# Kernel optimization log

Hardware: AMD Instinct MI355X
Metric: run time of the kernel (lower is better)

Reference implementation:

```python
import jax, jax.numpy as jnp
import numpy as np

B, T, D_MODEL = 256, 200, 2048
D_KEY, D_VAL = 128, 128


def setup_inputs() -> dict:
    key = jax.random.key(0)
    k_q, k_mask, k_wq, k_wk, k_wv = jax.random.split(key, 5)
    q = jax.random.normal(k_q, (B, T, D_MODEL), dtype=jnp.float32)
    pad_mask = jax.random.randint(k_mask, (B, 1, T), 0, 2, dtype=jnp.int32)
    # ensure key 0 is never padded so every causal row has >=1 valid key (no NaN softmax)
    pad_mask = pad_mask.at[:, :, 0].set(0)
    s = 1.0 / np.sqrt(D_MODEL)
    Wq = jax.random.normal(k_wq, (D_KEY, D_MODEL), dtype=jnp.float32) * s
    Wk = jax.random.normal(k_wk, (D_KEY, D_MODEL), dtype=jnp.float32) * s
    Wv = jax.random.normal(k_wv, (D_VAL, D_MODEL), dtype=jnp.float32) * s
    return {"q": q, "pad_mask": pad_mask, "Wq": Wq, "Wk": Wk, "Wv": Wv}


def reference(q, pad_mask, Wq, Wk, Wv):
    # self-attention: kv = q
    T_ = q.shape[1]
    C = q.shape[-1]  # note: original scales by d_model, not d_key
    Q = jnp.einsum('btc,kc->btk', q, Wq)   # [B,T,d_key]
    K = jnp.einsum('btc,kc->btk', q, Wk)   # [B,T,d_key]
    V = jnp.einsum('btc,vc->btv', q, Wv)   # [B,T,d_val]
    W = jnp.einsum('bqk,btk->bqt', Q, K) / jnp.sqrt(jnp.asarray(C, q.dtype))  # [B,T,T]
    tril = jnp.tril(jnp.ones((T_, T_), dtype=jnp.bool_))
    neg_inf = jnp.asarray(-jnp.inf, W.dtype)
    W = jnp.where(tril[None, :, :], W, neg_inf)          # causal mask
    W = jnp.where(pad_mask == 1, neg_inf, W)             # padding mask (broadcast [B,1,T])
    W = jax.nn.softmax(W, axis=-1)
    # dropout p=0.0 / eval mode -> identity
    return jnp.einsum('bqt,btv->bqv', W, V)              # [B,T,d_val]
```

## Files before the change

kernel.cpp:

```cpp
#include <hip/hip_runtime.h>

typedef __bf16 bf16x8 __attribute__((ext_vector_type(8)));
typedef __bf16 bf16x4 __attribute__((ext_vector_type(4)));
typedef float  f32x4  __attribute__((ext_vector_type(4)));

#define MFMA16(a,b,c) __builtin_amdgcn_mfma_f32_16x16x32_bf16((a),(b),(c),0,0,0)

constexpr int B_ = 256, T_ = 200, DM = 2048, DK = 128;
constexpr int VT_STRIDE = 208;

constexpr size_t OFF_W = 0;
constexpr size_t OFF_Q = 1572864;
constexpr size_t OFF_K = OFF_Q + 13107200;
constexpr size_t OFF_V = OFF_K + 13107200;

#define GLOAD_LDS16(G, L)                                                     \
  __builtin_amdgcn_global_load_lds(                                           \
      (const __attribute__((address_space(1))) void*)(G),                     \
      (__attribute__((address_space(3))) void*)(L), 16, 0, 0)

__global__ __launch_bounds__(256) void wconv_kernel(const float* __restrict__ Wq,
                                                    const float* __restrict__ Wk,
                                                    const float* __restrict__ Wv,
                                                    __bf16* __restrict__ Wcat) {
  int idx = (blockIdx.x * 256 + threadIdx.x) * 4;
  int sel = idx >> 18;
  const float* base = (sel == 0) ? Wq : (sel == 1) ? Wk : Wv;
  float4 f = *(const float4*)(base + (idx - (sel << 18)));
  bf16x4 o;
  o[0] = (__bf16)f.x; o[1] = (__bf16)f.y; o[2] = (__bf16)f.z; o[3] = (__bf16)f.w;
  *(bf16x4*)(Wcat + idx) = o;
}

__global__ __launch_bounds__(256) void proj_kernel(const float* __restrict__ q,
                                                   const __bf16* __restrict__ Wcat,
                                                   __bf16* __restrict__ Qo,
                                                   __bf16* __restrict__ Ko,
                                                   __bf16* __restrict__ Vt) {
  __shared__ alignas(16) char smem[65536];

  const int tid  = threadIdx.x;
  const int lane = tid & 63;
  const int wn   = tid >> 6;
  const int lhi  = lane >> 4, llo = lane & 15;
  const int m0   = blockIdx.x * 64;

  f32x4 acc[4][6];
#pragma unroll
  for (int i = 0; i < 4; ++i)
#pragma unroll
    for (int j = 0; j < 6; ++j) acc[i][j] = {0.f, 0.f, 0.f, 0.f};

  const float* agbase = q + (size_t)(m0 + (tid >> 3)) * DM
                          + (((tid & 7) ^ ((tid >> 3) & 7)) << 2);
  const __bf16* bgbase = Wcat + (size_t)(tid >> 2) * DM
                              + (((tid & 3) ^ ((tid >> 3) & 3)) << 3);

#define STAGE(BUF, K0)                                                        \
  {                                                                           \
    char* la = smem + (BUF) * 32768;                                          \
    char* lb = la + 8192;                                                     \
    _Pragma("unroll")                                                         \
    for (int r = 0; r < 2; ++r)                                               \
      GLOAD_LDS16(agbase + (size_t)r * 32 * DM + (K0), la + tid * 16 + r * 4096); \
    _Pragma("unroll")                                                         \
    for (int r = 0; r < 6; ++r)                                               \
      GLOAD_LDS16(bgbase + (size_t)r * 64 * DM + (K0), lb + tid * 16 + r * 4096); \
  }

#define COMPUTE(BUF)                                                          \
  {                                                                           \
    const char* la = smem + (BUF) * 32768;                                    \
    const char* lb = la + 8192;                                               \
    bf16x8 af[4];                                                             \
    _Pragma("unroll")                                                         \
    for (int i = 0; i < 4; ++i) {                                             \
      const int row = i * 16 + llo;                                           \
      f32x4 u = *(const f32x4*)(la + row * 128 + (((2 * lhi) ^ (llo & 7)) << 4));     \
      f32x4 v = *(const f32x4*)(la + row * 128 + (((2 * lhi + 1) ^ (llo & 7)) << 4)); \
      af[i][0]=(__bf16)u[0]; af[i][1]=(__bf16)u[1]; af[i][2]=(__bf16)u[2]; af[i][3]=(__bf16)u[3]; \
      af[i][4]=(__bf16)v[0]; af[i][5]=(__bf16)v[1]; af[i][6]=(__bf16)v[2]; af[i][7]=(__bf16)v[3]; \
    }                                                                         \
    bf16x8 bfr[6];                                                            \
    _Pragma("unroll")                                                         \
    for (int j = 0; j < 6; ++j) {                                             \
      const int row = wn * 96 + j * 16 + llo;                                 \
      bfr[j] = *(const bf16x8*)(lb + row * 64 + ((lhi ^ ((llo >> 1) & 3)) << 4)); \
    }                                                                         \
    _Pragma("unroll")                                                         \
    for (int i = 0; i < 4; ++i)                                               \
      _Pragma("unroll")                                                       \
      for (int j = 0; j < 6; ++j) acc[i][j] = MFMA16(af[i], bfr[j], acc[i][j]); \
  }

  constexpr int NK = DM / 32;
  STAGE(0, 0);
  __syncthreads();

  int buf = 0;
  for (int it = 0; it < NK; ++it) {
    if (it + 1 < NK) STAGE(buf ^ 1, (it + 1) * 32);
    COMPUTE(buf);
    __syncthreads();
    buf ^= 1;
  }
#undef STAGE
#undef COMPUTE

#pragma unroll
  for (int i = 0; i < 4; ++i) {
#pragma unroll
    for (int r = 0; r < 4; ++r) {
      int row = m0 + i * 16 + lhi * 4 + r;
      int b = row / 200;
      int t = row - b * 200;
#pragma unroll
      for (int j = 0; j < 6; ++j) {
        int col = wn * 96 + j * 16 + llo;
        __bf16 bv = (__bf16)acc[i][j][r];
        if (col < 128)       Qo[(size_t)row * DK + col] = bv;
        else if (col < 256)  Ko[(size_t)row * DK + (col - 128)] = bv;
        else                 Vt[((size_t)b * DK + (col - 256)) * VT_STRIDE + t] = bv;
      }
    }
  }
}

template <int QB>
__global__ __launch_bounds__(256, 1) void attn_kernel(const __bf16* __restrict__ Qg,
                                                      const __bf16* __restrict__ Kg,
                                                      const __bf16* __restrict__ Vt,
                                                      const int* __restrict__ padm,
                                                      float* __restrict__ out) {
  constexpr int Q0     = QB * 64;
  constexpr int KMAX   = (Q0 + 64 < T_) ? (Q0 + 64) : T_;
  constexpr int KTILES = (KMAX + 15) / 16;
  constexpr int KCC    = (KMAX + 31) / 32;
  constexpr int KT16   = KTILES * 16;
  constexpr int KP     = KCC * 32;
  constexpr int VS     = KP + 8;

  __shared__ __bf16 sK[KT16][136];
  __shared__ __bf16 sV[128][VS];
  __shared__ __bf16 sP[4][16][VS];
  __shared__ float  sMask[KT16];

  const int tid  = threadIdx.x;
  const int lane = tid & 63;
  const int w    = tid >> 6;
  const int b    = blockIdx.x;
  const int lhi  = lane >> 4, llo = lane & 15;

  for (int t = tid; t < KT16; t += 256) {
    float mv = -1e30f;
    if (t < KMAX && padm[b * T_ + t] == 0) mv = 0.0f;
    sMask[t] = mv;
  }
  for (int cid = tid; cid < KT16 * 16; cid += 256) {
    int t = cid >> 4, c = (cid & 15) * 8;
    int tg = (t < T_) ? t : (T_ - 1);
    *(bf16x8*)&sK[t][c] = *(const bf16x8*)(Kg + ((size_t)b * T_ + tg) * DK + c);
  }
  {
    constexpr int NCH = KP / 8;
    for (int cid = tid; cid < 128 * NCH; cid += 256) {
      int v = cid / NCH, t0 = (cid % NCH) * 8;
      bf16x8 val;
      if (t0 < VT_STRIDE) {
        val = *(const bf16x8*)(Vt + ((size_t)b * DK + v) * VT_STRIDE + t0);
      } else {
#pragma unroll
        for (int jz = 0; jz < 8; ++jz) val[jz] = (__bf16)0.0f;
      }
      *(bf16x8*)&sV[v][t0] = val;
    }
  }
  if constexpr (KT16 < KP) {
    constexpr int NC = (KP - KT16) / 8;
    for (int idx = tid; idx < 4 * 16 * NC; idx += 256) {
      int ww = idx / (16 * NC);
      int rem = idx % (16 * NC);
      int row = rem / NC, cc = (rem % NC) * 8;
      bf16x8 z;
#pragma unroll
      for (int jz = 0; jz < 8; ++jz) z[jz] = (__bf16)0.0f;
      *(bf16x8*)&sP[ww][row][KT16 + cc] = z;
    }
  }
  __syncthreads();

  const int q0w = Q0 + w * 16;
  bf16x8 qf[4];
  {
    int qrow = q0w + llo;
    if (qrow > T_ - 1) qrow = T_ - 1;
    const __bf16* qp = Qg + ((size_t)b * T_ + qrow) * DK + lhi * 8;
#pragma unroll
    for (int kk = 0; kk < 4; ++kk) qf[kk] = *(const bf16x8*)(qp + kk * 32);
  }

  float sc[KTILES][4];
  const float scale = 0.022097086912079608f;
#pragma unroll
  for (int tt = 0; tt < KTILES; ++tt) {
    f32x4 s = {0.f, 0.f, 0.f, 0.f};
    const __bf16* kp = &sK[tt * 16 + llo][lhi * 8];
#pragma unroll
    for (int kk = 0; kk < 4; ++kk) {
      bf16x8 kf = *(const bf16x8*)(kp + kk * 32);
      s = MFMA16(qf[kk], kf, s);
    }
    const int t = tt * 16 + llo;
    const float madd = sMask[t];
#pragma unroll
    for (int r = 0; r < 4; ++r) {
      int qq = q0w + lhi * 4 + r;
      float v = fmaf(s[r], scale, madd);
      sc[tt][r] = (t > qq) ? -1e30f : v;
    }
  }

#pragma unroll
  for (int r = 0; r < 4; ++r) {
    float mm = -3e38f;
#pragma unroll
    for (int tt = 0; tt < KTILES; ++tt) mm = fmaxf(mm, sc[tt][r]);
#pragma unroll
    for (int off = 1; off < 16; off <<= 1) mm = fmaxf(mm, __shfl_xor(mm, off));
    float ss = 0.f;
#pragma unroll
    for (int tt = 0; tt < KTILES; ++tt) { float e = __expf(sc[tt][r] - mm); sc[tt][r] = e; ss += e; }
#pragma unroll
    for (int off = 1; off < 16; off <<= 1) ss += __shfl_xor(ss, off);
    float inv = 1.0f / ss;
#pragma unroll
    for (int tt = 0; tt < KTILES; ++tt) sc[tt][r] *= inv;
  }

#pragma unroll
  for (int tt = 0; tt < KTILES; ++tt) {
    int t = tt * 16 + llo;
#pragma unroll
    for (int r = 0; r < 4; ++r) sP[w][lhi * 4 + r][t] = (__bf16)sc[tt][r];
  }
  __syncthreads();

  f32x4 oacc[8];
#pragma unroll
  for (int vt = 0; vt < 8; ++vt) oacc[vt] = {0.f, 0.f, 0.f, 0.f};
#pragma unroll
  for (int kc = 0; kc < KCC; ++kc) {
    bf16x8 pa = *(const bf16x8*)&sP[w][llo][kc * 32 + lhi * 8];
#pragma unroll
    for (int vt = 0; vt < 8; ++vt) {
      bf16x8 vb = *(const bf16x8*)&sV[vt * 16 + llo][kc * 32 + lhi * 8];
      oacc[vt] = MFMA16(pa, vb, oacc[vt]);
    }
  }

#pragma unroll
  for (int vt = 0; vt < 8; ++vt) {
#pragma unroll
    for (int r = 0; r < 4; ++r) {
      int qq = q0w + lhi * 4 + r;
      if (qq < T_) out[((size_t)b * T_ + qq) * DK + vt * 16 + llo] = oacc[vt][r];
    }
  }
}

extern "C" void kernel_launch(void* const* d_in, const int* in_sizes, int n_in,
                              void* d_out, int out_size, void* d_ws, size_t ws_size,
                              hipStream_t stream) {
  const float* q    = (const float*)d_in[0];
  const int*   padm = (const int*)d_in[1];
  const float* Wq   = (const float*)d_in[2];
  const float* Wk   = (const float*)d_in[3];
  const float* Wv   = (const float*)d_in[4];
  float* out        = (float*)d_out;

  char* ws = (char*)d_ws;
  __bf16* Wcat = (__bf16*)(ws + OFF_W);
  __bf16* Qb   = (__bf16*)(ws + OFF_Q);
  __bf16* Kb   = (__bf16*)(ws + OFF_K);
  __bf16* Vtb  = (__bf16*)(ws + OFF_V);

  wconv_kernel<<<768, 256, 0, stream>>>(Wq, Wk, Wv, Wcat);
  proj_kernel<<<800, 256, 0, stream>>>(q, Wcat, Qb, Kb, Vtb);
  attn_kernel<0><<<256, 256, 0, stream>>>(Qb, Kb, Vtb, padm, out);
  attn_kernel<1><<<256, 256, 0, stream>>>(Qb, Kb, Vtb, padm, out);
  attn_kernel<2><<<256, 256, 0, stream>>>(Qb, Kb, Vtb, padm, out);
  attn_kernel<3><<<256, 256, 0, stream>>>(Qb, Kb, Vtb, padm, out);
}
```

Before: 259.8 us.

## Enlarge projection tile to 128 rows and triple-buffer loads with vmcnt waits

The projection GEMM now uses 512-thread blocks covering 128 rows, with 8 waves in a 2x4 layout, so each staged weight tile is shared by twice as many output rows. The K loop moves from double to triple buffering: two stages are prefetched and explicit s_waitcnt vmcnt plus raw barriers keep loads in flight during compute. The aim is to cut redundant weight traffic and hide global-to-LDS latency. The cost is about 120 KB of LDS per block, which limits occupancy to one block per CU, and the hand-tuned vmcnt counts must match the number of loads issued per stage.

```diff
diff --git a/kernel.cpp b/kernel.cpp
--- a/kernel.cpp
+++ b/kernel.cpp
@@ -32,18 +32,19 @@
   *(bf16x4*)(Wcat + idx) = o;
 }
 
-__global__ __launch_bounds__(256) void proj_kernel(const float* __restrict__ q,
+__global__ __launch_bounds__(512) void proj_kernel(const float* __restrict__ q,
                                                    const __bf16* __restrict__ Wcat,
                                                    __bf16* __restrict__ Qo,
                                                    __bf16* __restrict__ Ko,
                                                    __bf16* __restrict__ Vt) {
-  __shared__ alignas(16) char smem[65536];
+  __shared__ alignas(16) char smem[122880];
 
   const int tid  = threadIdx.x;
   const int lane = tid & 63;
-  const int wn   = tid >> 6;
+  const int w    = tid >> 6;
+  const int wm   = w >> 2, wn = w & 3;
   const int lhi  = lane >> 4, llo = lane & 15;
-  const int m0   = blockIdx.x * 64;
+  const int m0   = blockIdx.x * 128;
 
   f32x4 acc[4][6];
 #pragma unroll
@@ -56,28 +57,28 @@
   const __bf16* bgbase = Wcat + (size_t)(tid >> 2) * DM
                               + (((tid & 3) ^ ((tid >> 3) & 3)) << 3);
 
-#define STAGE(BUF, K0)                                                        \
+#define STAGE(LB, K0)                                                         \
   {                                                                           \
-    char* la = smem + (BUF) * 32768;                                          \
-    char* lb = la + 8192;                                                     \
+    char* la_ = (LB);                                                         \
+    char* lb_ = la_ + 16384;                                                  \
     _Pragma("unroll")                                                         \
     for (int r = 0; r < 2; ++r)                                               \
-      GLOAD_LDS16(agbase + (size_t)r * 32 * DM + (K0), la + tid * 16 + r * 4096); \
-    _Pragma("unroll")                                                         \
-    for (int r = 0; r < 6; ++r)                                               \
-      GLOAD_LDS16(bgbase + (size_t)r * 64 * DM + (K0), lb + tid * 16 + r * 4096); \
-  }
-
-#define COMPUTE(BUF)                                                          \
+      GLOAD_LDS16(agbase + (size_t)r * 64 * DM + (K0), la_ + tid * 16 + r * 8192); \
+    _Pragma("unroll")                                                         \
+    for (int r = 0; r < 3; ++r)                                               \
+      GLOAD_LDS16(bgbase + (size_t)r * 128 * DM + (K0), lb_ + tid * 16 + r * 8192); \
+  }
+
+#define COMPUTE(LB)                                                           \
   {                                                                           \
-    const char* la = smem + (BUF) * 32768;                                    \
-    const char* lb = la + 8192;                                               \
+    const char* la_ = (LB);                                                   \
+    const char* lb_ = la_ + 16384;                                            \
     bf16x8 af[4];                                                             \
     _Pragma("unroll")                                                         \
     for (int i = 0; i < 4; ++i) {                                             \
-      const int row = i * 16 + llo;                                           \
-      f32x4 u = *(const f32x4*)(la + row * 128 + (((2 * lhi) ^ (llo & 7)) << 4));     \
-      f32x4 v = *(const f32x4*)(la + row * 128 + (((2 * lhi + 1) ^ (llo & 7)) << 4)); \
+      const int row = wm * 64 + i * 16 + llo;                                 \
+      f32x4 u = *(const f32x4*)(la_ + row * 128 + (((2 * lhi) ^ (llo & 7)) << 4));     \
+      f32x4 v = *(const f32x4*)(la_ + row * 128 + (((2 * lhi + 1) ^ (llo & 7)) << 4)); \
       af[i][0]=(__bf16)u[0]; af[i][1]=(__bf16)u[1]; af[i][2]=(__bf16)u[2]; af[i][3]=(__bf16)u[3]; \
       af[i][4]=(__bf16)v[0]; af[i][5]=(__bf16)v[1]; af[i][6]=(__bf16)v[2]; af[i][7]=(__bf16)v[3]; \
     }                                                                         \
@@ -85,7 +86,7 @@
     _Pragma("unroll")                                                         \
     for (int j = 0; j < 6; ++j) {                                             \
       const int row = wn * 96 + j * 16 + llo;                                 \
-      bfr[j] = *(const bf16x8*)(lb + row * 64 + ((lhi ^ ((llo >> 1) & 3)) << 4)); \
+      bfr[j] = *(const bf16x8*)(lb_ + row * 64 + ((lhi ^ ((llo >> 1) & 3)) << 4)); \
     }                                                                         \
     _Pragma("unroll")                                                         \
     for (int i = 0; i < 4; ++i)                                               \
@@ -94,15 +95,27 @@
   }
 
   constexpr int NK = DM / 32;
-  STAGE(0, 0);
-  __syncthreads();
-
-  int buf = 0;
-  for (int it = 0; it < NK; ++it) {
-    if (it + 1 < NK) STAGE(buf ^ 1, (it + 1) * 32);
-    COMPUTE(buf);
-    __syncthreads();
-    buf ^= 1;
+  STAGE(smem, 0);
+  STAGE(smem + 40960, 32);
+
+  int cur = 0;
+  for (int t = 0; t < NK; ++t) {
+    if (t + 2 < NK) {
+      int sb = cur + 2; if (sb >= 3) sb -= 3;
+      STAGE(smem + sb * 40960, (t + 2) * 32);
+      asm volatile("s_waitcnt vmcnt(10)" ::: "memory");
+      __builtin_amdgcn_s_barrier();
+    } else if (t + 2 == NK) {
+      asm volatile("s_waitcnt vmcnt(5)" ::: "memory");
+      __builtin_amdgcn_s_barrier();
+    } else {
+      asm volatile("s_waitcnt vmcnt(0)" ::: "memory");
+      __builtin_amdgcn_s_barrier();
+    }
+    COMPUTE(smem + cur * 40960);
+    asm volatile("s_waitcnt lgkmcnt(0)" ::: "memory");
+    __builtin_amdgcn_s_barrier();
+    cur = cur + 1; if (cur >= 3) cur -= 3;
   }
 #undef STAGE
 #undef COMPUTE
@@ -111,7 +124,7 @@
   for (int i = 0; i < 4; ++i) {
 #pragma unroll
     for (int r = 0; r < 4; ++r) {
-      int row = m0 + i * 16 + lhi * 4 + r;
+      int row = m0 + wm * 64 + i * 16 + lhi * 4 + r;
       int b = row / 200;
       int t = row - b * 200;
 #pragma unroll
@@ -285,7 +298,7 @@
   __bf16* Vtb  = (__bf16*)(ws + OFF_V);
 
   wconv_kernel<<<768, 256, 0, stream>>>(Wq, Wk, Wv, Wcat);
-  proj_kernel<<<800, 256, 0, stream>>>(q, Wcat, Qb, Kb, Vtb);
+  proj_kernel<<<400, 512, 0, stream>>>(q, Wcat, Qb, Kb, Vtb);
   attn_kernel<0><<<256, 256, 0, stream>>>(Qb, Kb, Vtb, padm, out);
   attn_kernel<1><<<256, 256, 0, stream>>>(Qb, Kb, Vtb, padm, out);
   attn_kernel<2><<<256, 256, 0, stream>>>(Qb, Kb, Vtb, padm, out);
```

Measured after the change: 232.2 us. -10.6%, faster.
